# Kernel optimization log

Measured on AMD Instinct MI355X. Metric: run time of the kernel, lower is better.

Reference implementation:

```python
import jax, jax.numpy as jnp
import numpy as np

B, C, IN, H = 64, 128, 1024, 512  # batch, channels, input features (=='seq_length' arg), hidden


def setup_inputs() -> dict:
    key = jax.random.key(0)
    ks = jax.random.split(key, 9)
    s = 1.0 / np.sqrt(H)  # PyTorch LSTM init: U(-1/sqrt(H), 1/sqrt(H))
    u = lambda k, shape: jax.random.uniform(k, shape, jnp.float32, -s, s)
    return {
        "x": jax.random.normal(ks[0], (B, C, IN), jnp.float32),
        # layer 0: one weight set per direction (fwd, bwd)
        "W_ih0": u(ks[1], (2, 4 * H, IN)),
        "W_hh0": u(ks[2], (2, 4 * H, H)),
        "b_ih0": u(ks[3], (2, 4 * H)),
        "b_hh0": u(ks[4], (2, 4 * H)),
        # layers 1..2: input is concat of both directions (2H)
        "W_ih12": u(ks[5], (2, 2, 4 * H, 2 * H)),
        "W_hh12": u(ks[6], (2, 2, 4 * H, H)),
        "b_ih12": u(ks[7], (2, 2, 4 * H)),
        "b_hh12": u(ks[8], (2, 2, 4 * H)),
    }


def _cell(inp, W_ih, b_ih, b_hh):
    # One LSTM step from zero state (h0 = c0 = 0): W_hh @ h0 == 0, f*c0 == 0.
    gates = inp @ W_ih.T + b_ih + b_hh  # [N, 4H]
    i, f, g, o = jnp.split(gates, 4, axis=-1)  # PyTorch gate order: i, f, g, o
    c = jax.nn.sigmoid(i) * jnp.tanh(g)
    return jax.nn.sigmoid(o) * jnp.tanh(c)  # h, shape [N, H]


def reference(x, W_ih0, W_hh0, b_ih0, b_hh0, W_ih12, W_hh12, b_ih12, b_hh12):
    b, c, n = x.shape
    # Each channel is an independent seq-len-1 LSTM call with zero init state,
    # so fold channels into the batch dimension. W_hh* contribute nothing (h0=0).
    xb = x.reshape(b * c, n)
    h = jnp.concatenate(
        [_cell(xb, W_ih0[d], b_ih0[d], b_hh0[d]) for d in range(2)], axis=-1
    )  # [b*c, 2H]
    for l in range(2):  # layers 1 and 2
        h = jnp.concatenate(
            [_cell(h, W_ih12[l, d], b_ih12[l, d], b_hh12[l, d]) for d in range(2)],
            axis=-1,
        )
    return h.reshape(b, c, 2 * H)  # [batch, channels, 2*hidden]
```

## Files before the change

### kernel.cpp

```cpp
#include <hip/hip_runtime.h>


typedef float f32x4 __attribute__((ext_vector_type(4)));
typedef short short8 __attribute__((ext_vector_type(8)));
typedef unsigned short u16;

#define NP 3072
#define MROWS 8192
#define KDIM 1024
#define BM 256
#define BN 192
#define BK 64
#define LDS_A_SZ (BM * BK * 2)
#define LDS_B_SZ (BN * BK * 2)
#define LDS_B_OFF (2 * LDS_A_SZ)

__device__ __forceinline__ u16 f2bf(float f) {
  unsigned u = __float_as_uint(f);
  u += 0x7fffu + ((u >> 16) & 1u);
  return (u16)(u >> 16);
}
__device__ __forceinline__ float sigmoid_f(float x) {
  return 1.0f / (1.0f + __expf(-x));
}
__device__ __forceinline__ float tanh_f(float x) {
  float xc = fminf(fmaxf(x, -15.0f), 15.0f);
  float e = __expf(2.0f * xc);
  return (e - 1.0f) / (e + 1.0f);
}
__device__ __forceinline__ void gload_lds16(const void* g, void* l) {
  __builtin_amdgcn_global_load_lds((const __attribute__((address_space(1))) void*)g,
                                   (__attribute__((address_space(3))) void*)l,
                                   16, 0, 0);
}


__global__ __launch_bounds__(256) void k_convert_x(const float* __restrict__ x,
                                                   u16* __restrict__ out) {
  int tid = blockIdx.x * 256 + threadIdx.x;
  const float4* src = (const float4*)x + (size_t)tid * 2;
  float4 v0 = src[0], v1 = src[1];
  union { u16 u[8]; uint4 v; } r;
  r.u[0] = f2bf(v0.x); r.u[1] = f2bf(v0.y); r.u[2] = f2bf(v0.z); r.u[3] = f2bf(v0.w);
  r.u[4] = f2bf(v1.x); r.u[5] = f2bf(v1.y); r.u[6] = f2bf(v1.z); r.u[7] = f2bf(v1.w);
  ((uint4*)out)[tid] = r.v;
}

__global__ __launch_bounds__(256) void k_pack_w(const float* __restrict__ Wih0,
                                                const float* __restrict__ Wih12,
                                                u16* __restrict__ P) {
  int tid = blockIdx.x * 256 + threadIdx.x;
  int s   = tid / (NP * 128);
  int rem = tid - s * (NP * 128);
  int p   = rem >> 7;
  int k8  = rem & 127;
  int hb = p / 48;
  int pr = p - hb * 48;
  int gs = pr >> 4;
  int hl = pr & 15;
  int hcol = hb * 16 + hl;
  int dir = hcol >> 9;
  int h   = hcol & 511;
  int og  = (gs == 0) ? 0 : (gs + 1);
  const float* src;
  if (s == 0)
    src = Wih0 + ((size_t)(dir * 2048 + og * 512 + h)) * 1024 + k8 * 8;
  else
    src = Wih12 + ((size_t)(((s - 1) * 2 + dir) * 2048 + og * 512 + h)) * 1024 + k8 * 8;
  float4 v0 = ((const float4*)src)[0];
  float4 v1 = ((const float4*)src)[1];
  union { u16 u[8]; uint4 v; } r;
  r.u[0] = f2bf(v0.x); r.u[1] = f2bf(v0.y); r.u[2] = f2bf(v0.z); r.u[3] = f2bf(v0.w);
  r.u[4] = f2bf(v1.x); r.u[5] = f2bf(v1.y); r.u[6] = f2bf(v1.z); r.u[7] = f2bf(v1.w);
  ((uint4*)P)[tid] = r.v;
}

__global__ __launch_bounds__(256) void k_pack_bias(const float* __restrict__ bih0,
                                                   const float* __restrict__ bhh0,
                                                   const float* __restrict__ bih12,
                                                   const float* __restrict__ bhh12,
                                                   float* __restrict__ pb) {
  int tid = blockIdx.x * 256 + threadIdx.x;
  if (tid >= 3 * NP) return;
  int s = tid / NP;
  int p = tid - s * NP;
  int hb = p / 48;
  int pr = p - hb * 48;
  int gs = pr >> 4;
  int hl = pr & 15;
  int hcol = hb * 16 + hl;
  int dir = hcol >> 9;
  int h   = hcol & 511;
  int og  = (gs == 0) ? 0 : (gs + 1);
  int j   = og * 512 + h;
  float v;
  if (s == 0) {
    int i = dir * 2048 + j;
    v = bih0[i] + bhh0[i];
  } else {
    int i = ((s - 1) * 2 + dir) * 2048 + j;
    v = bih12[i] + bhh12[i];
  }
  pb[tid] = v;
}


#define BAR()    __builtin_amdgcn_s_barrier()
#define SCHEDB() __builtin_amdgcn_sched_barrier(0)
#define WAITV(N) asm volatile("s_waitcnt vmcnt(" #N ")" ::: "memory")
#define MM(Macc, Aop, Bop) Macc = __builtin_amdgcn_mfma_f32_16x16x32_bf16(Aop, Bop, Macc, 0, 0, 0)

#define LDA(MQ, K32, M4, BUF) \
  (*(const short8*)(lds + ((K32) ? aK1 : aK0) + ((BUF) * LDS_A_SZ + (MQ) * 8192 + (M4) * 2048)))
#define LDB(N3, K32, BUF) \
  (*(const short8*)(lds + ((K32) ? bK1 : bK0) + ((BUF) * LDS_B_SZ + (N3) * 2048)))

#define STAGE_B(RB, BUF, KT) \
  gload_lds16(srcB + (size_t)(RB) * 64 * KDIM + (size_t)(KT) * BK, \
              lds + LDS_B_OFF + (BUF) * LDS_B_SZ + (RB) * 8192 + t * 16)
#define STAGE_A(ROWB, BUF, KT) \
  gload_lds16(srcA + (size_t)(ROWB) * KDIM + (size_t)(KT) * BK, \
              lds + (BUF) * LDS_A_SZ + (ROWB) * 128 + t * 16)

#define MM12(MQ, AA0, AA1, AA2, AA3, BB0, BB1, BB2) \
  MM(acc[(MQ)*4+0][0], AA0, BB0); MM(acc[(MQ)*4+1][0], AA1, BB0); \
  MM(acc[(MQ)*4+2][0], AA2, BB0); MM(acc[(MQ)*4+3][0], AA3, BB0); \
  MM(acc[(MQ)*4+0][1], AA0, BB1); MM(acc[(MQ)*4+1][1], AA1, BB1); \
  MM(acc[(MQ)*4+2][1], AA2, BB1); MM(acc[(MQ)*4+3][1], AA3, BB1); \
  MM(acc[(MQ)*4+0][2], AA0, BB2); MM(acc[(MQ)*4+1][2], AA1, BB2); \
  MM(acc[(MQ)*4+2][2], AA2, BB2); MM(acc[(MQ)*4+3][2], AA3, BB2);

#define TILE2(BUF, KT, DO_STAGE, LASTMID) \
  { \
     \
    a0 = LDA(0, 0, 0, BUF); a1 = LDA(0, 0, 1, BUF); a2 = LDA(0, 0, 2, BUF); a3 = LDA(0, 0, 3, BUF); \
    b00 = LDB(0, 0, BUF); b01 = LDB(1, 0, BUF); b02 = LDB(2, 0, BUF); \
    a4 = LDA(0, 1, 0, BUF); a5 = LDA(0, 1, 1, BUF); a6 = LDA(0, 1, 2, BUF); a7 = LDA(0, 1, 3, BUF); \
    b10 = LDB(0, 1, BUF); b11 = LDB(1, 1, BUF); b12 = LDB(2, 1, BUF); \
    if (DO_STAGE) { STAGE_B(0, (BUF)^1, (KT)+1); STAGE_B(1, (BUF)^1, (KT)+1); STAGE_B(2, (BUF)^1, (KT)+1); \
                    STAGE_A(0, (BUF)^1, (KT)+1); STAGE_A(128, (BUF)^1, (KT)+1); } \
    BAR(); \
    __builtin_amdgcn_s_setprio(1); \
    MM12(0, a0, a1, a2, a3, b00, b01, b02); \
    MM12(0, a4, a5, a6, a7, b10, b11, b12); \
    __builtin_amdgcn_s_setprio(0); \
    if (LASTMID) { WAITV(0); } else { WAITV(5); } \
    BAR(); SCHEDB(); \
     \
    a0 = LDA(1, 0, 0, BUF); a1 = LDA(1, 0, 1, BUF); a2 = LDA(1, 0, 2, BUF); a3 = LDA(1, 0, 3, BUF); \
    a4 = LDA(1, 1, 0, BUF); a5 = LDA(1, 1, 1, BUF); a6 = LDA(1, 1, 2, BUF); a7 = LDA(1, 1, 3, BUF); \
    if (DO_STAGE) { STAGE_A(64, (BUF)^1, (KT)+1); STAGE_A(192, (BUF)^1, (KT)+1); } \
    BAR(); \
    __builtin_amdgcn_s_setprio(1); \
    MM12(1, a0, a1, a2, a3, b00, b01, b02); \
    MM12(1, a4, a5, a6, a7, b10, b11, b12); \
    __builtin_amdgcn_s_setprio(0); \
    if (DO_STAGE) { WAITV(2); } \
    BAR(); SCHEDB(); \
  }

template <bool F32OUT>
__global__ __launch_bounds__(512, 2) void k_lstm_gemm8(const u16* __restrict__ A,
                                                       const u16* __restrict__ Bp,
                                                       const float* __restrict__ bias,
                                                       void* __restrict__ outp) {
  __shared__ __align__(16) char lds[114688];
  const int t    = threadIdx.x;
  const int lane = t & 63;
  const int w    = t >> 6;
  const int wr   = w >> 2;
  const int wc   = w & 3;
  const int r16  = lane & 15, kg = lane >> 4;

  const int n_hw = blockIdx.y * gridDim.x + blockIdx.x;
  const int c    = n_hw & 7;
  const int wlc  = n_hw >> 3;
  const int bx   = (c & 1) * 8 + (wlc & 7);
  const int by   = (c >> 1) * 8 + (wlc >> 3);
  const int brow = by * BM;
  const int bn0  = bx * BN;

  const int sw    = r16 & 7;
  const int slot0 = kg ^ sw;
  const int aK0 = wr * 16384 + r16 * 128 + slot0 * 16;
  const int aK1 = wr * 16384 + r16 * 128 + (slot0 ^ 4) * 16;
  const int bK0 = LDS_B_OFF + (wc * 48 + r16) * 128 + slot0 * 16;
  const int bK1 = LDS_B_OFF + (wc * 48 + r16) * 128 + (slot0 ^ 4) * 16;

  const int rr   = t >> 3;
  const int koct = ((t & 7) ^ (rr & 7)) << 3;
  const u16* srcA = A  + (size_t)(brow + rr) * KDIM + koct;
  const u16* srcB = Bp + (size_t)(bn0  + rr) * KDIM + koct;

  f32x4 acc[8][3];
#pragma unroll
  for (int m = 0; m < 8; ++m)
#pragma unroll
    for (int n = 0; n < 3; ++n) acc[m][n] = (f32x4){0.f, 0.f, 0.f, 0.f};

  short8 a0, a1, a2, a3, a4, a5, a6, a7, b00, b01, b02, b10, b11, b12;

  STAGE_B(0, 0, 0); STAGE_B(1, 0, 0); STAGE_B(2, 0, 0);
  STAGE_A(0, 0, 0); STAGE_A(128, 0, 0);
  STAGE_A(64, 0, 0); STAGE_A(192, 0, 0);
  WAITV(2);
  BAR(); SCHEDB();

  for (int k2 = 0; k2 < 7; ++k2) {
    int kt = k2 * 2;
    TILE2(0, kt, 1, 0);
    TILE2(1, kt + 1, 1, 0);
  }
  TILE2(0, 14, 1, 0);
  TILE2(1, 15, 0, 1);

  {
    int pb = bn0 + wc * 48;
    float biV = bias[pb + r16];
    float bgV = bias[pb + 16 + r16];
    float boV = bias[pb + 32 + r16];
    int hcol = (bx * 4 + wc) * 16 + r16;
#pragma unroll
    for (int m8 = 0; m8 < 8; ++m8) {
      int rowb = brow + wr * 128 + (m8 >> 2) * 64 + (m8 & 3) * 16 + kg * 4;
#pragma unroll
      for (int r = 0; r < 4; ++r) {
        float vi = acc[m8][0][r] + biV;
        float vg = acc[m8][1][r] + bgV;
        float vo = acc[m8][2][r] + boV;
        float c2 = sigmoid_f(vi) * tanh_f(vg);
        float hv = sigmoid_f(vo) * tanh_f(c2);
        size_t oidx = (size_t)(rowb + r) * 1024 + hcol;
        if (F32OUT) ((float*)outp)[oidx] = hv;
        else        ((u16*)outp)[oidx]   = f2bf(hv);
      }
    }
  }
}

extern "C" void kernel_launch(void* const* d_in, const int* in_sizes, int n_in,
                              void* d_out, int out_size, void* d_ws, size_t ws_size,
                              hipStream_t stream) {
  const float* x     = (const float*)d_in[0];
  const float* Wih0  = (const float*)d_in[1];
  const float* bih0  = (const float*)d_in[3];
  const float* bhh0  = (const float*)d_in[4];
  const float* Wih12 = (const float*)d_in[5];
  const float* bih12 = (const float*)d_in[7];
  const float* bhh12 = (const float*)d_in[8];

  char* ws = (char*)d_ws;
  u16*   xbf = (u16*)ws;
  u16*   h1  = (u16*)(ws + 16777216);
  u16*   h2  = (u16*)(ws + 33554432);
  u16*   P3  = (u16*)(ws + 50331648);
  float* pb3 = (float*)(ws + 69206016);

  k_convert_x<<<4096, 256, 0, stream>>>(x, xbf);
  k_pack_w<<<4608, 256, 0, stream>>>(Wih0, Wih12, P3);
  k_pack_bias<<<36, 256, 0, stream>>>(bih0, bhh0, bih12, bhh12, pb3);

  dim3 grid(NP / BN, MROWS / BM);
  k_lstm_gemm8<false><<<grid, 512, 0, stream>>>(xbf, P3, pb3, h1);
  k_lstm_gemm8<false><<<grid, 512, 0, stream>>>(h1, P3 + (size_t)NP * KDIM, pb3 + NP, h2);
  k_lstm_gemm8<true ><<<grid, 512, 0, stream>>>(h2, P3 + (size_t)2 * NP * KDIM, pb3 + 2 * NP, d_out);
}
```

Before: 202.3 us.

## Collapse two-phase K-tile schedule into single phase with one barrier per tile

Result: faster. 197.3 us (-2.5%).

```diff
diff --git a/kernel.cpp b/kernel.cpp
--- a/kernel.cpp
+++ b/kernel.cpp
@@ -130,32 +130,25 @@
   MM(acc[(MQ)*4+0][2], AA0, BB2); MM(acc[(MQ)*4+1][2], AA1, BB2); \
   MM(acc[(MQ)*4+2][2], AA2, BB2); MM(acc[(MQ)*4+3][2], AA3, BB2);
 
-#define TILE2(BUF, KT, DO_STAGE, LASTMID) \
+#define TILE1(BUF, KT, DO_STAGE) \
   { \
-     \
+    if (DO_STAGE) { STAGE_B(0, (BUF)^1, (KT)+1); STAGE_B(1, (BUF)^1, (KT)+1); STAGE_B(2, (BUF)^1, (KT)+1); \
+                    STAGE_A(0, (BUF)^1, (KT)+1); STAGE_A(128, (BUF)^1, (KT)+1); \
+                    STAGE_A(64, (BUF)^1, (KT)+1); STAGE_A(192, (BUF)^1, (KT)+1); } \
+    SCHEDB(); \
     a0 = LDA(0, 0, 0, BUF); a1 = LDA(0, 0, 1, BUF); a2 = LDA(0, 0, 2, BUF); a3 = LDA(0, 0, 3, BUF); \
     b00 = LDB(0, 0, BUF); b01 = LDB(1, 0, BUF); b02 = LDB(2, 0, BUF); \
+    a8 = LDA(1, 0, 0, BUF); a9 = LDA(1, 0, 1, BUF); aA = LDA(1, 0, 2, BUF); aB = LDA(1, 0, 3, BUF); \
     a4 = LDA(0, 1, 0, BUF); a5 = LDA(0, 1, 1, BUF); a6 = LDA(0, 1, 2, BUF); a7 = LDA(0, 1, 3, BUF); \
     b10 = LDB(0, 1, BUF); b11 = LDB(1, 1, BUF); b12 = LDB(2, 1, BUF); \
-    if (DO_STAGE) { STAGE_B(0, (BUF)^1, (KT)+1); STAGE_B(1, (BUF)^1, (KT)+1); STAGE_B(2, (BUF)^1, (KT)+1); \
-                    STAGE_A(0, (BUF)^1, (KT)+1); STAGE_A(128, (BUF)^1, (KT)+1); } \
-    BAR(); \
+    aC = LDA(1, 1, 0, BUF); aD = LDA(1, 1, 1, BUF); aE = LDA(1, 1, 2, BUF); aF = LDA(1, 1, 3, BUF); \
     __builtin_amdgcn_s_setprio(1); \
     MM12(0, a0, a1, a2, a3, b00, b01, b02); \
+    MM12(1, a8, a9, aA, aB, b00, b01, b02); \
     MM12(0, a4, a5, a6, a7, b10, b11, b12); \
+    MM12(1, aC, aD, aE, aF, b10, b11, b12); \
     __builtin_amdgcn_s_setprio(0); \
-    if (LASTMID) { WAITV(0); } else { WAITV(5); } \
-    BAR(); SCHEDB(); \
-     \
-    a0 = LDA(1, 0, 0, BUF); a1 = LDA(1, 0, 1, BUF); a2 = LDA(1, 0, 2, BUF); a3 = LDA(1, 0, 3, BUF); \
-    a4 = LDA(1, 1, 0, BUF); a5 = LDA(1, 1, 1, BUF); a6 = LDA(1, 1, 2, BUF); a7 = LDA(1, 1, 3, BUF); \
-    if (DO_STAGE) { STAGE_A(64, (BUF)^1, (KT)+1); STAGE_A(192, (BUF)^1, (KT)+1); } \
-    BAR(); \
-    __builtin_amdgcn_s_setprio(1); \
-    MM12(1, a0, a1, a2, a3, b00, b01, b02); \
-    MM12(1, a4, a5, a6, a7, b10, b11, b12); \
-    __builtin_amdgcn_s_setprio(0); \
-    if (DO_STAGE) { WAITV(2); } \
+    WAITV(0); \
     BAR(); SCHEDB(); \
   }
 
@@ -198,21 +191,22 @@
 #pragma unroll
     for (int n = 0; n < 3; ++n) acc[m][n] = (f32x4){0.f, 0.f, 0.f, 0.f};
 
-  short8 a0, a1, a2, a3, a4, a5, a6, a7, b00, b01, b02, b10, b11, b12;
+  short8 a0, a1, a2, a3, a4, a5, a6, a7, a8, a9, aA, aB, aC, aD, aE, aF;
+  short8 b00, b01, b02, b10, b11, b12;
 
   STAGE_B(0, 0, 0); STAGE_B(1, 0, 0); STAGE_B(2, 0, 0);
   STAGE_A(0, 0, 0); STAGE_A(128, 0, 0);
   STAGE_A(64, 0, 0); STAGE_A(192, 0, 0);
-  WAITV(2);
+  WAITV(0);
   BAR(); SCHEDB();
 
   for (int k2 = 0; k2 < 7; ++k2) {
     int kt = k2 * 2;
-    TILE2(0, kt, 1, 0);
-    TILE2(1, kt + 1, 1, 0);
-  }
-  TILE2(0, 14, 1, 0);
-  TILE2(1, 15, 0, 1);
+    TILE1(0, kt, 1);
+    TILE1(1, kt + 1, 1);
+  }
+  TILE1(0, 14, 1);
+  TILE1(1, 15, 0);
 
   {
     int pb = bn0 + wc * 48;
```
